# Kernel optimization log

Hardware: AMD Instinct MI355X
Metric: run time of the kernel (lower is better)

Reference implementation:

```python
import jax, jax.numpy as jnp
import numpy as np

N = 100000
E = 1600000
H = 128
G = 64  # num graphs


def setup_inputs() -> dict:
    key = jax.random.key(0)
    ks = jax.random.split(key, 20)
    s = 1.0 / np.sqrt(H)
    inp = {
        'x': jax.random.normal(ks[0], (N,), jnp.float32),
        'edge_index': jax.random.randint(ks[1], (2, E), 0, N, jnp.int32),
        'edge_attr': jax.random.normal(ks[2], (E, 1), jnp.float32),
        'batch': jnp.sort(jax.random.randint(ks[3], (N,), 0, G, jnp.int32)),
        # node/edge encoders (Linear(1, H))
        'ne_w': jax.random.normal(ks[4], (1, H), jnp.float32),
        'ne_b': jnp.zeros((H,), jnp.float32),
        'ee_w': jax.random.normal(ks[5], (1, H), jnp.float32),
        'ee_b': jnp.zeros((H,), jnp.float32),
        # conv1: internal edge lin (Linear(H,H)) + MLP (H->H->H)
        'lin1_w': jax.random.normal(ks[6], (H, H), jnp.float32) * s,
        'lin1_b': jnp.zeros((H,), jnp.float32),
        'w11': jax.random.normal(ks[7], (H, H), jnp.float32) * s,
        'b11': jnp.zeros((H,), jnp.float32),
        'w12': jax.random.normal(ks[8], (H, H), jnp.float32) * s,
        'b12': jnp.zeros((H,), jnp.float32),
        # conv2
        'lin2_w': jax.random.normal(ks[9], (H, H), jnp.float32) * s,
        'lin2_b': jnp.zeros((H,), jnp.float32),
        'w21': jax.random.normal(ks[10], (H, H), jnp.float32) * s,
        'b21': jnp.zeros((H,), jnp.float32),
        'w22': jax.random.normal(ks[11], (H, H), jnp.float32) * s,
        'b22': jnp.zeros((H,), jnp.float32),
    }
    return inp


def _gine(h, edge_index, e, lin_w, lin_b, w1, b1, w2, b2, eps=0.0):
    # message: ReLU(x_j + Lin(edge_attr)), aggregated (sum) at target nodes
    src, dst = edge_index[0], edge_index[1]
    m = jax.nn.relu(h[src] + e @ lin_w + lin_b)           # [E, H]
    agg = jax.ops.segment_sum(m, dst, num_segments=N)      # [N, H]
    z = (1.0 + eps) * h + agg
    return jax.nn.relu(z @ w1 + b1) @ w2 + b2


def reference(x, edge_index, edge_attr, batch, ne_w, ne_b, ee_w, ee_b,
              lin1_w, lin1_b, w11, b11, w12, b12,
              lin2_w, lin2_b, w21, b21, w22, b22):
    h = x.reshape(-1, 1) @ ne_w + ne_b                     # [N, H]
    e = edge_attr @ ee_w + ee_b                            # [E, H]
    h = jax.nn.relu(_gine(h, edge_index, e, lin1_w, lin1_b, w11, b11, w12, b12))
    h = jax.nn.relu(_gine(h, edge_index, e, lin2_w, lin2_b, w21, b21, w22, b22))
    # global mean pool per graph
    sums = jax.ops.segment_sum(h, batch, num_segments=G)   # [G, H]
    cnt = jax.ops.segment_sum(jnp.ones((N,), h.dtype), batch, num_segments=G)
    return sums / jnp.maximum(cnt, 1.0)[:, None]
```

## Files before the change

kernel.cpp:

```cpp
#include <hip/hip_runtime.h>

typedef unsigned short u16;
typedef unsigned int u32;
typedef __bf16 bfrag __attribute__((ext_vector_type(8)));
typedef float f32x4 __attribute__((ext_vector_type(4)));
typedef float f32x2 __attribute__((ext_vector_type(2)));

__device__ __forceinline__ u16 f2bf(float f) {
    u32 u = __float_as_uint(f);
    u32 r = (u + 0x7FFFu + ((u >> 16) & 1u)) >> 16;
    return (u16)r;
}
__device__ __forceinline__ float bf2f(u32 h) {
    return __uint_as_float(h << 16);
}

__global__ __launch_bounds__(1024) void prepack_bcount_kernel(
    const int* __restrict__ dst, int* __restrict__ bcnt, int* __restrict__ done,
    int* __restrict__ bstart, int* __restrict__ bcur, int E, int nb, int nbc,
    const float* __restrict__ w11, const float* __restrict__ w12,
    const float* __restrict__ w21, const float* __restrict__ w22,
    u16* __restrict__ hi, u16* __restrict__ lo,
    const float* __restrict__ ne_b, const float* __restrict__ ee_w, const float* __restrict__ ee_b,
    const float* __restrict__ lin1_w, const float* __restrict__ lin1_b,
    const float* __restrict__ lin2_w, const float* __restrict__ lin2_b,
    float* __restrict__ u1, float* __restrict__ C1, float* __restrict__ u2, float* __restrict__ C2)
{
    if (blockIdx.x >= (u32)nbc) {
        int pb = blockIdx.x - nbc;
        if (pb == 64) {
            int c = threadIdx.x;
            if (c < 128) {
                float s1 = 0.f, t1 = 0.f, s2 = 0.f, t2 = 0.f;
                for (int k = 0; k < 128; ++k) {
                    float w1 = lin1_w[k * 128 + c];
                    float w2 = lin2_w[k * 128 + c];
                    float ew = ee_w[k], eb = ee_b[k];
                    s1 = fmaf(ew, w1, s1); t1 = fmaf(eb, w1, t1);
                    s2 = fmaf(ew, w2, s2); t2 = fmaf(eb, w2, t2);
                }
                u1[c] = s1; C1[c] = t1 + lin1_b[c] + ne_b[c];
                u2[c] = s2; C2[c] = t2 + lin2_b[c];
            }
            return;
        }
        int which = pb >> 4;
        const float* w = (which == 0) ? w11 : (which == 1) ? w12 : (which == 2) ? w21 : w22;
        int o = (pb & 15) * 1024 + threadIdx.x;
        int j = o & 7;
        int lane = (o >> 3) & 63;
        int ct = (o >> 9) & 7;
        int ks = o >> 12;
        int k = ks * 32 + ((lane >> 4) * 8) + j;
        int c = ct * 16 + (lane & 15);
        float v = w[k * 128 + c];
        u16 h = f2bf(v);
        float vh = bf2f(h);
        u16 l = f2bf(v - vh);
        hi[which * 16384 + o] = h;
        lo[which * 16384 + o] = l;
        return;
    }

    __shared__ int h[256];
    __shared__ int is_last;
    if (threadIdx.x < 256) h[threadIdx.x] = 0;
    __syncthreads();
    int idx = blockIdx.x * 1024 + threadIdx.x;
    int e = idx * 4;
    if (e + 3 < E) {
        int4 d4 = ((const int4*)dst)[idx];
        atomicAdd(&h[d4.x >> 9], 1);
        atomicAdd(&h[d4.y >> 9], 1);
        atomicAdd(&h[d4.z >> 9], 1);
        atomicAdd(&h[d4.w >> 9], 1);
    } else {
        for (int k = e; k < E; ++k) atomicAdd(&h[dst[k] >> 9], 1);
    }
    __syncthreads();
    if (threadIdx.x < 256 && h[threadIdx.x]) atomicAdd(&bcnt[threadIdx.x], h[threadIdx.x]);
    __syncthreads();
    if (threadIdx.x == 0) {
        __threadfence();
        is_last = (atomicAdd(done, 1) == nbc - 1);
    }
    __syncthreads();
    if (!is_last) return;
    if (threadIdx.x < 256) h[threadIdx.x] = atomicAdd(&bcnt[threadIdx.x], 0);
    __syncthreads();
    __shared__ int excl[256];
    if (threadIdx.x < 64) {
        int l = threadIdx.x;
        int v0 = h[4 * l], v1 = h[4 * l + 1], v2 = h[4 * l + 2], v3 = h[4 * l + 3];
        int tot = v0 + v1 + v2 + v3;
        int run = tot;
#pragma unroll
        for (int off = 1; off < 64; off <<= 1) {
            int t = __shfl_up(run, off);
            if (l >= off) run += t;
        }
        int ex = run - tot;
        excl[4 * l] = ex;
        excl[4 * l + 1] = ex + v0;
        excl[4 * l + 2] = ex + v0 + v1;
        excl[4 * l + 3] = ex + v0 + v1 + v2;
    }
    __syncthreads();
    if (threadIdx.x < nb) {
        int ex = excl[threadIdx.x];
        bstart[threadIdx.x] = ex;
        bcur[threadIdx.x] = ex;
        if (threadIdx.x == nb - 1) bstart[nb] = ex + h[threadIdx.x];
    }
}

__global__ __launch_bounds__(1024) void bin_kernel(
    const int* __restrict__ src, const int* __restrict__ dst, const float* __restrict__ eattr,
    int* __restrict__ bucket_cursor,
    int2* __restrict__ binned, int E, int nb)
{
    __shared__ int hist[256];
    __shared__ int basel[256];
    __shared__ int gbase[256];
    __shared__ int2 stage[4096];
    __shared__ unsigned char sb[4096];
    const int tid = threadIdx.x;
    const int e0 = blockIdx.x * 4096;
    const int valid = min(4096, E - e0);

    if (tid < 256) hist[tid] = 0;
    __syncthreads();

    int d[4], s[4], a[4], rk[4];
    bool ok[4];
    const int eb = e0 + tid * 4;
    if (eb + 3 < E) {
        int4 d4 = *(const int4*)(dst + eb);
        int4 s4 = *(const int4*)(src + eb);
        int4 a4 = *(const int4*)((const int*)eattr + eb);
        d[0] = d4.x; d[1] = d4.y; d[2] = d4.z; d[3] = d4.w;
        s[0] = s4.x; s[1] = s4.y; s[2] = s4.z; s[3] = s4.w;
        a[0] = a4.x; a[1] = a4.y; a[2] = a4.z; a[3] = a4.w;
        ok[0] = ok[1] = ok[2] = ok[3] = true;
    } else {
#pragma unroll
        for (int k = 0; k < 4; ++k) {
            int e = eb + k;
            ok[k] = e < E;
            if (ok[k]) {
                d[k] = dst[e];
                s[k] = src[e];
                a[k] = __float_as_int(eattr[e]);
            }
        }
    }
#pragma unroll
    for (int k = 0; k < 4; ++k) {
        if (ok[k]) rk[k] = atomicAdd(&hist[d[k] >> 9], 1);
    }
    __syncthreads();
    if (tid < 64) {
        int l = tid;
        int v0 = hist[4 * l], v1 = hist[4 * l + 1], v2 = hist[4 * l + 2], v3 = hist[4 * l + 3];
        int tot = v0 + v1 + v2 + v3;
        int run = tot;
#pragma unroll
        for (int off = 1; off < 64; off <<= 1) {
            int t = __shfl_up(run, off);
            if (l >= off) run += t;
        }
        int ex = run - tot;
        basel[4 * l] = ex;
        basel[4 * l + 1] = ex + v0;
        basel[4 * l + 2] = ex + v0 + v1;
        basel[4 * l + 3] = ex + v0 + v1 + v2;
    }
    __syncthreads();
    if (tid < nb && hist[tid] > 0) gbase[tid] = atomicAdd(&bucket_cursor[tid], hist[tid]);
#pragma unroll
    for (int k = 0; k < 4; ++k) {
        if (ok[k]) {
            int b = d[k] >> 9;
            int pos = basel[b] + rk[k];
            stage[pos] = make_int2(s[k] | ((d[k] & 511) << 17), a[k]);
            sb[pos] = (unsigned char)b;
        }
    }
    __syncthreads();
    for (int i = tid; i < valid; i += 1024) {
        int b = (int)sb[i];
        binned[gbase[b] + (i - basel[b])] = stage[i];
    }
}

__global__ __launch_bounds__(1024) void fine_kernel(
    const int2* __restrict__ binned, const int* __restrict__ bstart,
    int* __restrict__ rowptr, int2* __restrict__ edges, int N, int nbuckets)
{
    __shared__ int hist[512];
    __shared__ int excl[512];
    const int tid = threadIdx.x;
    const int b = blockIdx.x;
    const int s0 = bstart[b], s1 = bstart[b + 1];
    if (tid < 512) hist[tid] = 0;
    __syncthreads();
    for (int i = s0 + tid; i < s1; i += 1024)
        atomicAdd(&hist[(binned[i].x >> 17) & 511], 1);
    __syncthreads();
    if (tid < 64) {
        int l = tid;
        int v[8], pre[8];
        int tot = 0;
#pragma unroll
        for (int k = 0; k < 8; ++k) { v[k] = hist[8 * l + k]; pre[k] = tot; tot += v[k]; }
        int run = tot;
#pragma unroll
        for (int off = 1; off < 64; off <<= 1) {
            int t = __shfl_up(run, off);
            if (l >= off) run += t;
        }
        int ex = run - tot;
#pragma unroll
        for (int k = 0; k < 8; ++k) excl[8 * l + k] = ex + pre[k];
    }
    __syncthreads();
    const int nbase = b << 9;
    if (tid < 512 && nbase + tid < N) rowptr[nbase + tid] = s0 + excl[tid];
    if (b == nbuckets - 1 && tid == 0) rowptr[N] = s1;
    __syncthreads();
    for (int i = s0 + tid; i < s1; i += 1024) {
        int2 ed = binned[i];
        int dlo = (ed.x >> 17) & 511;
        ed.x &= 0x1FFFF;
        int pos = atomicAdd(&excl[dlo], 1);
        edges[s0 + pos] = ed;
    }
}


__device__ __forceinline__ void p1_batch8(
    const float* __restrict__ x, const int2* __restrict__ edges, int j,
    f32x2 A, f32x2 Bv, f32x2 Cv, f32x2& acc)
{
    int2 ep = edges[j + (threadIdx.x & 7)];
    float xs[8], av[8];
#pragma unroll
    for (int t = 0; t < 8; ++t) {
        u32 s = (u32)__builtin_amdgcn_readlane(ep.x, t);
        av[t] = __int_as_float(__builtin_amdgcn_readlane(ep.y, t));
        xs[t] = *(const float*)((const char*)x + (s << 2));
    }
    const f32x2 zero = {0.f, 0.f};
#pragma unroll
    for (int t = 0; t < 8; ++t) {
        f32x2 m = __builtin_elementwise_fma((f32x2){xs[t], xs[t]}, A,
                    __builtin_elementwise_fma((f32x2){av[t], av[t]}, Bv, Cv));
        acc += __builtin_elementwise_max(m, zero);
    }
}

__device__ __forceinline__ void p1_batch8x2(
    const float* __restrict__ x, const int2* __restrict__ edges, int j0, int j1,
    f32x2 A, f32x2 Bv, f32x2 Cv, f32x2& acc0, f32x2& acc1)
{
    int2 ep0 = edges[j0 + (threadIdx.x & 7)];
    int2 ep1 = edges[j1 + (threadIdx.x & 7)];
    float xs0[8], av0[8], xs1[8], av1[8];
#pragma unroll
    for (int t = 0; t < 8; ++t) {
        u32 s = (u32)__builtin_amdgcn_readlane(ep0.x, t);
        av0[t] = __int_as_float(__builtin_amdgcn_readlane(ep0.y, t));
        xs0[t] = *(const float*)((const char*)x + (s << 2));
    }
#pragma unroll
    for (int t = 0; t < 8; ++t) {
        u32 s = (u32)__builtin_amdgcn_readlane(ep1.x, t);
        av1[t] = __int_as_float(__builtin_amdgcn_readlane(ep1.y, t));
        xs1[t] = *(const float*)((const char*)x + (s << 2));
    }
    const f32x2 zero = {0.f, 0.f};
#pragma unroll
    for (int t = 0; t < 8; ++t) {
        f32x2 m = __builtin_elementwise_fma((f32x2){xs0[t], xs0[t]}, A,
                    __builtin_elementwise_fma((f32x2){av0[t], av0[t]}, Bv, Cv));
        acc0 += __builtin_elementwise_max(m, zero);
    }
#pragma unroll
    for (int t = 0; t < 8; ++t) {
        f32x2 m = __builtin_elementwise_fma((f32x2){xs1[t], xs1[t]}, A,
                    __builtin_elementwise_fma((f32x2){av1[t], av1[t]}, Bv, Cv));
        acc1 += __builtin_elementwise_max(m, zero);
    }
}

__global__ __launch_bounds__(256) void pull1_kernel(
    const float* __restrict__ x,
    const int* __restrict__ rowptr, const int2* __restrict__ edges,
    const float* __restrict__ ne_w, const float* __restrict__ ne_b,
    const float* __restrict__ u1, const float* __restrict__ C1,
    u16* __restrict__ zb, int N)
{
    const int lane = threadIdx.x & 63;
    int pair = blockIdx.x * 4 + (threadIdx.x >> 6);
    int n0 = pair * 2;
    if (n0 >= N) return;
    const bool has1 = (n0 + 1 < N);
    f32x2 A   = *(const f32x2*)(ne_w + 2 * lane);
    f32x2 Bv  = *(const f32x2*)(u1   + 2 * lane);
    f32x2 Cv  = *(const f32x2*)(C1   + 2 * lane);
    f32x2 nbv = *(const f32x2*)(ne_b + 2 * lane);
    const f32x2 zero = {0.f, 0.f};
    int j0  = rowptr[n0];
    int je0 = rowptr[n0 + 1];
    int j1  = je0;
    int je1 = has1 ? rowptr[n0 + 2] : je0;
    float xn0 = x[n0];
    float xn1 = has1 ? x[n0 + 1] : 0.f;
    f32x2 acc0 = zero, acc1 = zero;
    while (j0 + 8 <= je0 && j1 + 8 <= je1) {
        p1_batch8x2(x, edges, j0, j1, A, Bv, Cv, acc0, acc1);
        j0 += 8; j1 += 8;
    }
    for (; j0 + 8 <= je0; j0 += 8) p1_batch8(x, edges, j0, A, Bv, Cv, acc0);
    for (; j1 + 8 <= je1; j1 += 8) p1_batch8(x, edges, j1, A, Bv, Cv, acc1);
    for (; j0 < je0; ++j0) {
        int2 ep = edges[j0];
        u32 s = (u32)__builtin_amdgcn_readfirstlane(ep.x);
        float av = __int_as_float(__builtin_amdgcn_readfirstlane(ep.y));
        float xs = *(const float*)((const char*)x + (s << 2));
        f32x2 m = __builtin_elementwise_fma((f32x2){xs, xs}, A,
                    __builtin_elementwise_fma((f32x2){av, av}, Bv, Cv));
        acc0 += __builtin_elementwise_max(m, zero);
    }
    for (; j1 < je1; ++j1) {
        int2 ep = edges[j1];
        u32 s = (u32)__builtin_amdgcn_readfirstlane(ep.x);
        float av = __int_as_float(__builtin_amdgcn_readfirstlane(ep.y));
        float xs = *(const float*)((const char*)x + (s << 2));
        f32x2 m = __builtin_elementwise_fma((f32x2){xs, xs}, A,
                    __builtin_elementwise_fma((f32x2){av, av}, Bv, Cv));
        acc1 += __builtin_elementwise_max(m, zero);
    }
    f32x2 z0 = __builtin_elementwise_fma((f32x2){xn0, xn0}, A, nbv) + acc0;
    ((u32*)(zb + (long)n0 * 128))[lane] = (u32)f2bf(z0.x) | ((u32)f2bf(z0.y) << 16);
    if (has1) {
        f32x2 z1 = __builtin_elementwise_fma((f32x2){xn1, xn1}, A, nbv) + acc1;
        ((u32*)(zb + (long)(n0 + 1) * 128))[lane] = (u32)f2bf(z1.x) | ((u32)f2bf(z1.y) << 16);
    }
}

__device__ __forceinline__ void p2_batch8(
    const u16* __restrict__ h1b, const int2* __restrict__ edges, int j,
    u32 loff, f32x2 Bv, f32x2 Cv, f32x2& acc)
{
    int2 ep = edges[j + (threadIdx.x & 7)];
    u32 hv[8];
    float av[8];
#pragma unroll
    for (int t = 0; t < 8; ++t) {
        u32 s = (u32)__builtin_amdgcn_readlane(ep.x, t);
        av[t] = __int_as_float(__builtin_amdgcn_readlane(ep.y, t));
        hv[t] = *(const u32*)((const char*)h1b + ((s << 8) | loff));
    }
    const f32x2 zero = {0.f, 0.f};
#pragma unroll
    for (int t = 0; t < 8; ++t) {
        f32x2 h = { __uint_as_float(hv[t] << 16), __uint_as_float(hv[t] & 0xFFFF0000u) };
        f32x2 m = h + __builtin_elementwise_fma((f32x2){av[t], av[t]}, Bv, Cv);
        acc += __builtin_elementwise_max(m, zero);
    }
}

__device__ __forceinline__ void p2_batch8x2(
    const u16* __restrict__ h1b, const int2* __restrict__ edges, int j0, int j1,
    u32 loff, f32x2 Bv, f32x2 Cv, f32x2& acc0, f32x2& acc1)
{
    int2 ep0 = edges[j0 + (threadIdx.x & 7)];
    int2 ep1 = edges[j1 + (threadIdx.x & 7)];
    u32 hv0[8], hv1[8];
    float av0[8], av1[8];
#pragma unroll
    for (int t = 0; t < 8; ++t) {
        u32 s = (u32)__builtin_amdgcn_readlane(ep0.x, t);
        av0[t] = __int_as_float(__builtin_amdgcn_readlane(ep0.y, t));
        hv0[t] = *(const u32*)((const char*)h1b + ((s << 8) | loff));
    }
#pragma unroll
    for (int t = 0; t < 8; ++t) {
        u32 s = (u32)__builtin_amdgcn_readlane(ep1.x, t);
        av1[t] = __int_as_float(__builtin_amdgcn_readlane(ep1.y, t));
        hv1[t] = *(const u32*)((const char*)h1b + ((s << 8) | loff));
    }
    const f32x2 zero = {0.f, 0.f};
#pragma unroll
    for (int t = 0; t < 8; ++t) {
        f32x2 h = { __uint_as_float(hv0[t] << 16), __uint_as_float(hv0[t] & 0xFFFF0000u) };
        f32x2 m = h + __builtin_elementwise_fma((f32x2){av0[t], av0[t]}, Bv, Cv);
        acc0 += __builtin_elementwise_max(m, zero);
    }
#pragma unroll
    for (int t = 0; t < 8; ++t) {
        f32x2 h = { __uint_as_float(hv1[t] << 16), __uint_as_float(hv1[t] & 0xFFFF0000u) };
        f32x2 m = h + __builtin_elementwise_fma((f32x2){av1[t], av1[t]}, Bv, Cv);
        acc1 += __builtin_elementwise_max(m, zero);
    }
}

__global__ __launch_bounds__(256) void pull2_kernel(
    const u16* __restrict__ h1b,
    const int* __restrict__ rowptr, const int2* __restrict__ edges,
    const float* __restrict__ u2, const float* __restrict__ C2,
    u16* __restrict__ zb2, int N)
{
    const int lane = threadIdx.x & 63;
    const int lane2 = 2 * lane;
    const u32 loff = (u32)lane2 * 2u;
    int pair = blockIdx.x * 4 + (threadIdx.x >> 6);
    int n0 = pair * 2;
    if (n0 >= N) return;
    const bool has1 = (n0 + 1 < N);
    f32x2 Bv = *(const f32x2*)(u2 + lane2);
    f32x2 Cv = *(const f32x2*)(C2 + lane2);
    const f32x2 zero = {0.f, 0.f};
    int j0  = rowptr[n0];
    int je0 = rowptr[n0 + 1];
    int j1  = je0;
    int je1 = has1 ? rowptr[n0 + 2] : je0;
    u32 hn0 = *(const u32*)((const char*)h1b + (((u32)n0 << 8) | loff));
    u32 hn1 = has1 ? *(const u32*)((const char*)h1b + (((u32)(n0 + 1) << 8) | loff)) : 0u;
    f32x2 acc0 = zero, acc1 = zero;
    while (j0 + 8 <= je0 && j1 + 8 <= je1) {
        p2_batch8x2(h1b, edges, j0, j1, loff, Bv, Cv, acc0, acc1);
        j0 += 8; j1 += 8;
    }
    for (; j0 + 8 <= je0; j0 += 8) p2_batch8(h1b, edges, j0, loff, Bv, Cv, acc0);
    for (; j1 + 8 <= je1; j1 += 8) p2_batch8(h1b, edges, j1, loff, Bv, Cv, acc1);
    for (; j0 < je0; ++j0) {
        int2 ep = edges[j0];
        u32 s = (u32)__builtin_amdgcn_readfirstlane(ep.x);
        float av = __int_as_float(__builtin_amdgcn_readfirstlane(ep.y));
        u32 hv = *(const u32*)((const char*)h1b + ((s << 8) | loff));
        f32x2 h = { __uint_as_float(hv << 16), __uint_as_float(hv & 0xFFFF0000u) };
        f32x2 m = h + __builtin_elementwise_fma((f32x2){av, av}, Bv, Cv);
        acc0 += __builtin_elementwise_max(m, zero);
    }
    for (; j1 < je1; ++j1) {
        int2 ep = edges[j1];
        u32 s = (u32)__builtin_amdgcn_readfirstlane(ep.x);
        float av = __int_as_float(__builtin_amdgcn_readfirstlane(ep.y));
        u32 hv = *(const u32*)((const char*)h1b + ((s << 8) | loff));
        f32x2 h = { __uint_as_float(hv << 16), __uint_as_float(hv & 0xFFFF0000u) };
        f32x2 m = h + __builtin_elementwise_fma((f32x2){av, av}, Bv, Cv);
        acc1 += __builtin_elementwise_max(m, zero);
    }
    f32x2 h0 = { __uint_as_float(hn0 << 16), __uint_as_float(hn0 & 0xFFFF0000u) };
    f32x2 z0 = h0 + acc0;
    ((u32*)(zb2 + (long)n0 * 128))[lane] = (u32)f2bf(z0.x) | ((u32)f2bf(z0.y) << 16);
    if (has1) {
        f32x2 h1 = { __uint_as_float(hn1 << 16), __uint_as_float(hn1 & 0xFFFF0000u) };
        f32x2 z1 = h1 + acc1;
        ((u32*)(zb2 + (long)(n0 + 1) * 128))[lane] = (u32)f2bf(z1.x) | ((u32)f2bf(z1.y) << 16);
    }
}

__global__ __launch_bounds__(256) void mlp_kernel(
    const u16* __restrict__ zb,
    const u16* __restrict__ w1hi, const u16* __restrict__ w1lo,
    const u16* __restrict__ w2hi, const u16* __restrict__ w2lo,
    const float* __restrict__ b1, const float* __restrict__ b2,
    u16* __restrict__ outb)
{
    __shared__ __align__(16) u16 tls[64][136];
    const int lane = threadIdx.x & 63;
    const int wv = threadIdx.x >> 6;
    const int m = lane & 15;
    const int q = lane >> 4;
    const int ko = q * 8;
    const long base_row = (long)blockIdx.x * 64;
    const int ct0 = wv * 2;

    f32x4 acc[2][4];
#pragma unroll
    for (int c = 0; c < 2; ++c)
#pragma unroll
        for (int g = 0; g < 4; ++g) acc[c][g] = (f32x4){0.f, 0.f, 0.f, 0.f};

#pragma unroll
    for (int ks = 0; ks < 4; ++ks) {
        bfrag a[4];
#pragma unroll
        for (int g = 0; g < 4; ++g)
            a[g] = *(const bfrag*)(zb + (base_row + g * 16 + m) * 128 + ks * 32 + ko);
#pragma unroll
        for (int c = 0; c < 2; ++c) {
            const int off = (((ks * 8 + ct0 + c) * 64) + lane) * 8;
            bfrag bh = *(const bfrag*)(w1hi + off);
            bfrag bl = *(const bfrag*)(w1lo + off);
#pragma unroll
            for (int g = 0; g < 4; ++g)
                acc[c][g] = __builtin_amdgcn_mfma_f32_16x16x32_bf16(a[g], bh, acc[c][g], 0, 0, 0);
#pragma unroll
            for (int g = 0; g < 4; ++g)
                acc[c][g] = __builtin_amdgcn_mfma_f32_16x16x32_bf16(a[g], bl, acc[c][g], 0, 0, 0);
        }
    }
#pragma unroll
    for (int c = 0; c < 2; ++c) {
        float bv = b1[(ct0 + c) * 16 + m];
#pragma unroll
        for (int g = 0; g < 4; ++g)
#pragma unroll
            for (int r = 0; r < 4; ++r) {
                float v = fmaxf(acc[c][g][r] + bv, 0.f);
                tls[g * 16 + q * 4 + r][(ct0 + c) * 16 + m] = f2bf(v);
            }
    }
    __syncthreads();

    f32x4 acc2[2][4];
#pragma unroll
    for (int c = 0; c < 2; ++c)
#pragma unroll
        for (int g = 0; g < 4; ++g) acc2[c][g] = (f32x4){0.f, 0.f, 0.f, 0.f};

#pragma unroll
    for (int ks = 0; ks < 4; ++ks) {
        bfrag a[4];
#pragma unroll
        for (int g = 0; g < 4; ++g)
            a[g] = *(const bfrag*)(&tls[g * 16 + m][ks * 32 + ko]);
#pragma unroll
        for (int c = 0; c < 2; ++c) {
            const int off = (((ks * 8 + ct0 + c) * 64) + lane) * 8;
            bfrag bh = *(const bfrag*)(w2hi + off);
            bfrag bl = *(const bfrag*)(w2lo + off);
#pragma unroll
            for (int g = 0; g < 4; ++g)
                acc2[c][g] = __builtin_amdgcn_mfma_f32_16x16x32_bf16(a[g], bh, acc2[c][g], 0, 0, 0);
#pragma unroll
            for (int g = 0; g < 4; ++g)
                acc2[c][g] = __builtin_amdgcn_mfma_f32_16x16x32_bf16(a[g], bl, acc2[c][g], 0, 0, 0);
        }
    }
    __syncthreads();
#pragma unroll
    for (int c = 0; c < 2; ++c) {
        float bv = b2[(ct0 + c) * 16 + m];
#pragma unroll
        for (int g = 0; g < 4; ++g)
#pragma unroll
            for (int r = 0; r < 4; ++r) {
                float v = fmaxf(acc2[c][g][r] + bv, 0.f);
                tls[g * 16 + q * 4 + r][(ct0 + c) * 16 + m] = f2bf(v);
            }
    }
    __syncthreads();
#pragma unroll
    for (int it = 0; it < 4; ++it) {
        int chunk = threadIdx.x + it * 256;
        int row = chunk >> 4;
        int c8 = (chunk & 15) * 8;
        *(uint4*)(outb + (base_row + row) * 128 + c8) = *(const uint4*)(&tls[row][c8]);
    }
}

__global__ __launch_bounds__(256) void mlp_pool_kernel(
    const u16* __restrict__ zb,
    const u16* __restrict__ w1hi, const u16* __restrict__ w1lo,
    const u16* __restrict__ w2hi, const u16* __restrict__ w2lo,
    const float* __restrict__ b1, const float* __restrict__ b2,
    const int* __restrict__ batch, float* __restrict__ poolacc, int N)
{
    __shared__ __align__(16) u16 tls[64][136];
    __shared__ int bsh[64];
    const int lane = threadIdx.x & 63;
    const int wv = threadIdx.x >> 6;
    const int m = lane & 15;
    const int q = lane >> 4;
    const int ko = q * 8;
    const long base_row = (long)blockIdx.x * 64;
    const int ct0 = wv * 2;

    if (threadIdx.x < 64) {
        long node = base_row + threadIdx.x;
        bsh[threadIdx.x] = (node < N) ? batch[node] : -1;
    }

    f32x4 acc[2][4];
#pragma unroll
    for (int c = 0; c < 2; ++c)
#pragma unroll
        for (int g = 0; g < 4; ++g) acc[c][g] = (f32x4){0.f, 0.f, 0.f, 0.f};

#pragma unroll
    for (int ks = 0; ks < 4; ++ks) {
        bfrag a[4];
#pragma unroll
        for (int g = 0; g < 4; ++g)
            a[g] = *(const bfrag*)(zb + (base_row + g * 16 + m) * 128 + ks * 32 + ko);
#pragma unroll
        for (int c = 0; c < 2; ++c) {
            const int off = (((ks * 8 + ct0 + c) * 64) + lane) * 8;
            bfrag bh = *(const bfrag*)(w1hi + off);
            bfrag bl = *(const bfrag*)(w1lo + off);
#pragma unroll
            for (int g = 0; g < 4; ++g)
                acc[c][g] = __builtin_amdgcn_mfma_f32_16x16x32_bf16(a[g], bh, acc[c][g], 0, 0, 0);
#pragma unroll
            for (int g = 0; g < 4; ++g)
                acc[c][g] = __builtin_amdgcn_mfma_f32_16x16x32_bf16(a[g], bl, acc[c][g], 0, 0, 0);
        }
    }
#pragma unroll
    for (int c = 0; c < 2; ++c) {
        float bv = b1[(ct0 + c) * 16 + m];
#pragma unroll
        for (int g = 0; g < 4; ++g)
#pragma unroll
            for (int r = 0; r < 4; ++r) {
                float v = fmaxf(acc[c][g][r] + bv, 0.f);
                tls[g * 16 + q * 4 + r][(ct0 + c) * 16 + m] = f2bf(v);
            }
    }
    __syncthreads();

    f32x4 acc2[2][4];
#pragma unroll
    for (int c = 0; c < 2; ++c)
#pragma unroll
        for (int g = 0; g < 4; ++g) acc2[c][g] = (f32x4){0.f, 0.f, 0.f, 0.f};

#pragma unroll
    for (int ks = 0; ks < 4; ++ks) {
        bfrag a[4];
#pragma unroll
        for (int g = 0; g < 4; ++g)
            a[g] = *(const bfrag*)(&tls[g * 16 + m][ks * 32 + ko]);
#pragma unroll
        for (int c = 0; c < 2; ++c) {
            const int off = (((ks * 8 + ct0 + c) * 64) + lane) * 8;
            bfrag bh = *(const bfrag*)(w2hi + off);
            bfrag bl = *(const bfrag*)(w2lo + off);
#pragma unroll
            for (int g = 0; g < 4; ++g)
                acc2[c][g] = __builtin_amdgcn_mfma_f32_16x16x32_bf16(a[g], bh, acc2[c][g], 0, 0, 0);
#pragma unroll
            for (int g = 0; g < 4; ++g)
                acc2[c][g] = __builtin_amdgcn_mfma_f32_16x16x32_bf16(a[g], bl, acc2[c][g], 0, 0, 0);
        }
    }
    __syncthreads();
#pragma unroll
    for (int c = 0; c < 2; ++c) {
        float bv = b2[(ct0 + c) * 16 + m];
#pragma unroll
        for (int g = 0; g < 4; ++g)
#pragma unroll
            for (int r = 0; r < 4; ++r) {
                float v = fmaxf(acc2[c][g][r] + bv, 0.f);
                tls[g * 16 + q * 4 + r][(ct0 + c) * 16 + m] = f2bf(v);
            }
    }
    __syncthreads();

    int c = threadIdx.x & 127;
    int half = threadIdx.x >> 7;
    int r0 = half * 32, r1 = r0 + 32;
    int cur = -1;
    float sum = 0.f;
    for (int r = r0; r < r1; ++r) {
        int g = bsh[r];
        if (g < 0) break;
        float v = bf2f((u32)tls[r][c]);
        if (g != cur) {
            if (cur >= 0) atomicAdd(&poolacc[cur * 128 + c], sum);
            sum = 0.f;
            cur = g;
        }
        sum += v;
    }
    if (cur >= 0) atomicAdd(&poolacc[cur * 128 + c], sum);
}

__global__ __launch_bounds__(128) void pool2_kernel(
    const float* __restrict__ acc, const int* __restrict__ batch,
    float* __restrict__ out, int n)
{
    int g = blockIdx.x;
    int c = threadIdx.x;
    int lo = 0, hi = n;
    while (lo < hi) { int mid = (lo + hi) >> 1; if (batch[mid] < g) lo = mid + 1; else hi = mid; }
    int s = lo;
    lo = s; hi = n;
    while (lo < hi) { int mid = (lo + hi) >> 1; if (batch[mid] < g + 1) lo = mid + 1; else hi = mid; }
    int cnt = lo - s;
    out[g * 128 + c] = acc[g * 128 + c] / (float)(cnt > 0 ? cnt : 1);
}

extern "C" void kernel_launch(void* const* d_in, const int* in_sizes, int n_in,
                              void* d_out, int out_size, void* d_ws, size_t ws_size,
                              hipStream_t stream)
{
    const float* x      = (const float*)d_in[0];
    const int*   ei     = (const int*)d_in[1];
    const float* eattr  = (const float*)d_in[2];
    const int*   batch  = (const int*)d_in[3];
    const float* ne_w   = (const float*)d_in[4];
    const float* ne_b   = (const float*)d_in[5];
    const float* ee_w   = (const float*)d_in[6];
    const float* ee_b   = (const float*)d_in[7];
    const float* lin1_w = (const float*)d_in[8];
    const float* lin1_b = (const float*)d_in[9];
    const float* w11    = (const float*)d_in[10];
    const float* b11    = (const float*)d_in[11];
    const float* w12    = (const float*)d_in[12];
    const float* b12    = (const float*)d_in[13];
    const float* lin2_w = (const float*)d_in[14];
    const float* lin2_b = (const float*)d_in[15];
    const float* w21    = (const float*)d_in[16];
    const float* b21    = (const float*)d_in[17];
    const float* w22    = (const float*)d_in[18];
    const float* b22    = (const float*)d_in[19];

    const int N = in_sizes[0];
    const int E = in_sizes[2];
    const int G = out_size / 128;
    const int Npad = ((N + 63) / 64) * 64;
    const int nb = (N + 511) >> 9;
    const int nbc = (E + 4095) / 4096;
    const int* esrc = ei;
    const int* edst = ei + E;

    char* p = (char*)d_ws;
    auto alloc = [&](size_t bytes) -> void* {
        void* r = (void*)p;
        p += (bytes + 255) & ~(size_t)255;
        return r;
    };
    float* u1 = (float*)alloc(128 * 4);
    float* C1 = (float*)alloc(128 * 4);
    float* u2 = (float*)alloc(128 * 4);
    float* C2 = (float*)alloc(128 * 4);
    int* bcnt   = (int*)alloc(1024);
    int* done   = (int*)alloc(256);
    float* poolacc = (float*)alloc((size_t)G * 128 * 4);
    int* bstart = (int*)alloc(((size_t)nb + 1) * 4);
    int* bcur   = (int*)alloc((size_t)nb * 4);
    int* rowptr = (int*)alloc(((size_t)N + 1) * 4);
    int2* edges = (int2*)alloc((size_t)E * 8);
    int2* binned = (int2*)alloc((size_t)E * 8);
    u16* whi = (u16*)alloc((size_t)4 * 16384 * 2);
    u16* wlo = (u16*)alloc((size_t)4 * 16384 * 2);
    u16* bufA = (u16*)alloc((size_t)Npad * 128 * 2);
    u16* bufB = (u16*)alloc((size_t)Npad * 128 * 2);

    size_t zbytes = (size_t)((char*)poolacc + (size_t)G * 128 * 4 - (char*)bcnt);
    hipMemsetAsync(bcnt, 0, zbytes, stream);

    prepack_bcount_kernel<<<nbc + 65, 1024, 0, stream>>>(
        edst, bcnt, done, bstart, bcur, E, nb, nbc,
        w11, w12, w21, w22, whi, wlo,
        ne_b, ee_w, ee_b, lin1_w, lin1_b, lin2_w, lin2_b, u1, C1, u2, C2);

    bin_kernel<<<nbc, 1024, 0, stream>>>(esrc, edst, eattr, bcur, binned, E, nb);
    fine_kernel<<<nb, 1024, 0, stream>>>(binned, bstart, rowptr, edges, N, nb);

    pull1_kernel<<<(N + 7) / 8, 256, 0, stream>>>(x, rowptr, edges, ne_w, ne_b, u1, C1,
                                                  bufA, N);
    mlp_kernel<<<Npad / 64, 256, 0, stream>>>(bufA, whi, wlo, whi + 16384, wlo + 16384,
                                              b11, b12, bufB);
    pull2_kernel<<<(N + 7) / 8, 256, 0, stream>>>(bufB, rowptr, edges, u2, C2, bufA, N);
    mlp_pool_kernel<<<Npad / 64, 256, 0, stream>>>(bufA, whi + 32768, wlo + 32768,
                                                   whi + 49152, wlo + 49152, b21, b22,
                                                   batch, poolacc, N);

    pool2_kernel<<<G, 128, 0, stream>>>(poolacc, batch, (float*)d_out, N);
}
```

Before: 320.8 us.

## Split each wavefront into two half-waves, one per node, with 4-wide features

The pull kernels now assign each half of a 64-lane wavefront to one of the two destination nodes. Each lane handles 4 features through 8-byte loads, where before every lane handled 2 features for both nodes. Edge indices are loaded per lane directly rather than broadcast with readlane, so the two halves gather different source rows in the same instruction. The intent is to double the bytes per gather load and remove the sequential two-node loop. The cost is wasted work when degrees differ: the inactive half still runs the tail iterations with its accumulation masked off.

New measurement: 370.0 us. 1.15x slower.

```diff
diff --git a/kernel.cpp b/kernel.cpp
--- a/kernel.cpp
+++ b/kernel.cpp
@@ -238,58 +238,34 @@
 }
 
 
-__device__ __forceinline__ void p1_batch8(
-    const float* __restrict__ x, const int2* __restrict__ edges, int j,
-    f32x2 A, f32x2 Bv, f32x2 Cv, f32x2& acc)
-{
-    int2 ep = edges[j + (threadIdx.x & 7)];
-    float xs[8], av[8];
+__device__ __forceinline__ f32x4 bf4(uint2 hv) {
+    f32x4 r;
+    r[0] = __uint_as_float(hv.x << 16);
+    r[1] = __uint_as_float(hv.x & 0xFFFF0000u);
+    r[2] = __uint_as_float(hv.y << 16);
+    r[3] = __uint_as_float(hv.y & 0xFFFF0000u);
+    return r;
+}
+
+__device__ __forceinline__ void p1_any8(
+    const float* __restrict__ x, const int2* __restrict__ edges, int jb,
+    f32x4 A, f32x4 Bv, f32x4 Cv, bool act, f32x4& acc)
+{
+    int2 ep[8];
+    float xs[8];
+#pragma unroll
+    for (int t = 0; t < 8; ++t) ep[t] = edges[jb + t];
+#pragma unroll
+    for (int t = 0; t < 8; ++t)
+        xs[t] = *(const float*)((const char*)x + (((u32)ep[t].x) << 2));
+    const f32x4 zero = {0.f, 0.f, 0.f, 0.f};
 #pragma unroll
     for (int t = 0; t < 8; ++t) {
-        u32 s = (u32)__builtin_amdgcn_readlane(ep.x, t);
-        av[t] = __int_as_float(__builtin_amdgcn_readlane(ep.y, t));
-        xs[t] = *(const float*)((const char*)x + (s << 2));
-    }
-    const f32x2 zero = {0.f, 0.f};
-#pragma unroll
-    for (int t = 0; t < 8; ++t) {
-        f32x2 m = __builtin_elementwise_fma((f32x2){xs[t], xs[t]}, A,
-                    __builtin_elementwise_fma((f32x2){av[t], av[t]}, Bv, Cv));
-        acc += __builtin_elementwise_max(m, zero);
-    }
-}
-
-__device__ __forceinline__ void p1_batch8x2(
-    const float* __restrict__ x, const int2* __restrict__ edges, int j0, int j1,
-    f32x2 A, f32x2 Bv, f32x2 Cv, f32x2& acc0, f32x2& acc1)
-{
-    int2 ep0 = edges[j0 + (threadIdx.x & 7)];
-    int2 ep1 = edges[j1 + (threadIdx.x & 7)];
-    float xs0[8], av0[8], xs1[8], av1[8];
-#pragma unroll
-    for (int t = 0; t < 8; ++t) {
-        u32 s = (u32)__builtin_amdgcn_readlane(ep0.x, t);
-        av0[t] = __int_as_float(__builtin_amdgcn_readlane(ep0.y, t));
-        xs0[t] = *(const float*)((const char*)x + (s << 2));
-    }
-#pragma unroll
-    for (int t = 0; t < 8; ++t) {
-        u32 s = (u32)__builtin_amdgcn_readlane(ep1.x, t);
-        av1[t] = __int_as_float(__builtin_amdgcn_readlane(ep1.y, t));
-        xs1[t] = *(const float*)((const char*)x + (s << 2));
-    }
-    const f32x2 zero = {0.f, 0.f};
-#pragma unroll
-    for (int t = 0; t < 8; ++t) {
-        f32x2 m = __builtin_elementwise_fma((f32x2){xs0[t], xs0[t]}, A,
-                    __builtin_elementwise_fma((f32x2){av0[t], av0[t]}, Bv, Cv));
-        acc0 += __builtin_elementwise_max(m, zero);
-    }
-#pragma unroll
-    for (int t = 0; t < 8; ++t) {
-        f32x2 m = __builtin_elementwise_fma((f32x2){xs1[t], xs1[t]}, A,
-                    __builtin_elementwise_fma((f32x2){av1[t], av1[t]}, Bv, Cv));
-        acc1 += __builtin_elementwise_max(m, zero);
+        float av = __int_as_float(ep[t].y);
+        f32x4 m = __builtin_elementwise_fma((f32x4){xs[t], xs[t], xs[t], xs[t]}, A,
+                    __builtin_elementwise_fma((f32x4){av, av, av, av}, Bv, Cv));
+        m = __builtin_elementwise_max(m, zero);
+        if (act) acc += m;
     }
 }
 
@@ -301,108 +277,76 @@
     u16* __restrict__ zb, int N)
 {
     const int lane = threadIdx.x & 63;
+    const int half = lane >> 5;
+    const int cl = lane & 31;
+    const u32 loff = (u32)cl * 8u;
     int pair = blockIdx.x * 4 + (threadIdx.x >> 6);
     int n0 = pair * 2;
     if (n0 >= N) return;
     const bool has1 = (n0 + 1 < N);
-    f32x2 A   = *(const f32x2*)(ne_w + 2 * lane);
-    f32x2 Bv  = *(const f32x2*)(u1   + 2 * lane);
-    f32x2 Cv  = *(const f32x2*)(C1   + 2 * lane);
-    f32x2 nbv = *(const f32x2*)(ne_b + 2 * lane);
-    const f32x2 zero = {0.f, 0.f};
+    f32x4 A   = *(const f32x4*)(ne_w + cl * 4);
+    f32x4 Bv  = *(const f32x4*)(u1   + cl * 4);
+    f32x4 Cv  = *(const f32x4*)(C1   + cl * 4);
+    f32x4 nbv = *(const f32x4*)(ne_b + cl * 4);
+    const f32x4 zero = {0.f, 0.f, 0.f, 0.f};
     int j0  = rowptr[n0];
     int je0 = rowptr[n0 + 1];
     int j1  = je0;
     int je1 = has1 ? rowptr[n0 + 2] : je0;
-    float xn0 = x[n0];
-    float xn1 = has1 ? x[n0 + 1] : 0.f;
-    f32x2 acc0 = zero, acc1 = zero;
+    const int nself = half ? (has1 ? n0 + 1 : n0) : n0;
+    float xn = x[nself];
+    f32x4 acc = zero;
     while (j0 + 8 <= je0 && j1 + 8 <= je1) {
-        p1_batch8x2(x, edges, j0, j1, A, Bv, Cv, acc0, acc1);
+        int jb = half ? j1 : j0;
+        p1_any8(x, edges, jb, A, Bv, Cv, true, acc);
         j0 += 8; j1 += 8;
     }
-    for (; j0 + 8 <= je0; j0 += 8) p1_batch8(x, edges, j0, A, Bv, Cv, acc0);
-    for (; j1 + 8 <= je1; j1 += 8) p1_batch8(x, edges, j1, A, Bv, Cv, acc1);
+    while (j0 + 8 <= je0) { p1_any8(x, edges, j0, A, Bv, Cv, half == 0, acc); j0 += 8; }
+    while (j1 + 8 <= je1) { p1_any8(x, edges, j1, A, Bv, Cv, half == 1, acc); j1 += 8; }
     for (; j0 < je0; ++j0) {
         int2 ep = edges[j0];
-        u32 s = (u32)__builtin_amdgcn_readfirstlane(ep.x);
-        float av = __int_as_float(__builtin_amdgcn_readfirstlane(ep.y));
-        float xs = *(const float*)((const char*)x + (s << 2));
-        f32x2 m = __builtin_elementwise_fma((f32x2){xs, xs}, A,
-                    __builtin_elementwise_fma((f32x2){av, av}, Bv, Cv));
-        acc0 += __builtin_elementwise_max(m, zero);
+        float xs = *(const float*)((const char*)x + (((u32)ep.x) << 2));
+        float av = __int_as_float(ep.y);
+        f32x4 m = __builtin_elementwise_fma((f32x4){xs, xs, xs, xs}, A,
+                    __builtin_elementwise_fma((f32x4){av, av, av, av}, Bv, Cv));
+        m = __builtin_elementwise_max(m, zero);
+        if (half == 0) acc += m;
     }
     for (; j1 < je1; ++j1) {
         int2 ep = edges[j1];
-        u32 s = (u32)__builtin_amdgcn_readfirstlane(ep.x);
-        float av = __int_as_float(__builtin_amdgcn_readfirstlane(ep.y));
-        float xs = *(const float*)((const char*)x + (s << 2));
-        f32x2 m = __builtin_elementwise_fma((f32x2){xs, xs}, A,
-                    __builtin_elementwise_fma((f32x2){av, av}, Bv, Cv));
-        acc1 += __builtin_elementwise_max(m, zero);
-    }
-    f32x2 z0 = __builtin_elementwise_fma((f32x2){xn0, xn0}, A, nbv) + acc0;
-    ((u32*)(zb + (long)n0 * 128))[lane] = (u32)f2bf(z0.x) | ((u32)f2bf(z0.y) << 16);
-    if (has1) {
-        f32x2 z1 = __builtin_elementwise_fma((f32x2){xn1, xn1}, A, nbv) + acc1;
-        ((u32*)(zb + (long)(n0 + 1) * 128))[lane] = (u32)f2bf(z1.x) | ((u32)f2bf(z1.y) << 16);
-    }
-}
-
-__device__ __forceinline__ void p2_batch8(
-    const u16* __restrict__ h1b, const int2* __restrict__ edges, int j,
-    u32 loff, f32x2 Bv, f32x2 Cv, f32x2& acc)
-{
-    int2 ep = edges[j + (threadIdx.x & 7)];
-    u32 hv[8];
-    float av[8];
+        float xs = *(const float*)((const char*)x + (((u32)ep.x) << 2));
+        float av = __int_as_float(ep.y);
+        f32x4 m = __builtin_elementwise_fma((f32x4){xs, xs, xs, xs}, A,
+                    __builtin_elementwise_fma((f32x4){av, av, av, av}, Bv, Cv));
+        m = __builtin_elementwise_max(m, zero);
+        if (half == 1) acc += m;
+    }
+    f32x4 z = __builtin_elementwise_fma((f32x4){xn, xn, xn, xn}, A, nbv) + acc;
+    uint2 outp;
+    outp.x = (u32)f2bf(z[0]) | ((u32)f2bf(z[1]) << 16);
+    outp.y = (u32)f2bf(z[2]) | ((u32)f2bf(z[3]) << 16);
+    if (half == 0 || has1)
+        *(uint2*)((char*)zb + (((u32)nself) << 8) + loff) = outp;
+}
+
+__device__ __forceinline__ void p2_any8(
+    const u16* __restrict__ h1b, const int2* __restrict__ edges, int jb, u32 loff,
+    f32x4 Bv, f32x4 Cv, bool act, f32x4& acc)
+{
+    int2 ep[8];
+    uint2 hv[8];
+#pragma unroll
+    for (int t = 0; t < 8; ++t) ep[t] = edges[jb + t];
+#pragma unroll
+    for (int t = 0; t < 8; ++t)
+        hv[t] = *(const uint2*)((const char*)h1b + ((((u32)ep[t].x) << 8) | loff));
+    const f32x4 zero = {0.f, 0.f, 0.f, 0.f};
 #pragma unroll
     for (int t = 0; t < 8; ++t) {
-        u32 s = (u32)__builtin_amdgcn_readlane(ep.x, t);
-        av[t] = __int_as_float(__builtin_amdgcn_readlane(ep.y, t));
-        hv[t] = *(const u32*)((const char*)h1b + ((s << 8) | loff));
-    }
-    const f32x2 zero = {0.f, 0.f};
-#pragma unroll
-    for (int t = 0; t < 8; ++t) {
-        f32x2 h = { __uint_as_float(hv[t] << 16), __uint_as_float(hv[t] & 0xFFFF0000u) };
-        f32x2 m = h + __builtin_elementwise_fma((f32x2){av[t], av[t]}, Bv, Cv);
-        acc += __builtin_elementwise_max(m, zero);
-    }
-}
-
-__device__ __forceinline__ void p2_batch8x2(
-    const u16* __restrict__ h1b, const int2* __restrict__ edges, int j0, int j1,
-    u32 loff, f32x2 Bv, f32x2 Cv, f32x2& acc0, f32x2& acc1)
-{
-    int2 ep0 = edges[j0 + (threadIdx.x & 7)];
-    int2 ep1 = edges[j1 + (threadIdx.x & 7)];
-    u32 hv0[8], hv1[8];
-    float av0[8], av1[8];
-#pragma unroll
-    for (int t = 0; t < 8; ++t) {
-        u32 s = (u32)__builtin_amdgcn_readlane(ep0.x, t);
-        av0[t] = __int_as_float(__builtin_amdgcn_readlane(ep0.y, t));
-        hv0[t] = *(const u32*)((const char*)h1b + ((s << 8) | loff));
-    }
-#pragma unroll
-    for (int t = 0; t < 8; ++t) {
-        u32 s = (u32)__builtin_amdgcn_readlane(ep1.x, t);
-        av1[t] = __int_as_float(__builtin_amdgcn_readlane(ep1.y, t));
-        hv1[t] = *(const u32*)((const char*)h1b + ((s << 8) | loff));
-    }
-    const f32x2 zero = {0.f, 0.f};
-#pragma unroll
-    for (int t = 0; t < 8; ++t) {
-        f32x2 h = { __uint_as_float(hv0[t] << 16), __uint_as_float(hv0[t] & 0xFFFF0000u) };
-        f32x2 m = h + __builtin_elementwise_fma((f32x2){av0[t], av0[t]}, Bv, Cv);
-        acc0 += __builtin_elementwise_max(m, zero);
-    }
-#pragma unroll
-    for (int t = 0; t < 8; ++t) {
-        f32x2 h = { __uint_as_float(hv1[t] << 16), __uint_as_float(hv1[t] & 0xFFFF0000u) };
-        f32x2 m = h + __builtin_elementwise_fma((f32x2){av1[t], av1[t]}, Bv, Cv);
-        acc1 += __builtin_elementwise_max(m, zero);
+        float av = __int_as_float(ep[t].y);
+        f32x4 m = bf4(hv[t]) + __builtin_elementwise_fma((f32x4){av, av, av, av}, Bv, Cv);
+        m = __builtin_elementwise_max(m, zero);
+        if (act) acc += m;
     }
 }
 
@@ -413,54 +357,52 @@
     u16* __restrict__ zb2, int N)
 {
     const int lane = threadIdx.x & 63;
-    const int lane2 = 2 * lane;
-    const u32 loff = (u32)lane2 * 2u;
+    const int half = lane >> 5;
+    const int cl = lane & 31;
+    const u32 loff = (u32)cl * 8u;
     int pair = blockIdx.x * 4 + (threadIdx.x >> 6);
     int n0 = pair * 2;
     if (n0 >= N) return;
     const bool has1 = (n0 + 1 < N);
-    f32x2 Bv = *(const f32x2*)(u2 + lane2);
-    f32x2 Cv = *(const f32x2*)(C2 + lane2);
-    const f32x2 zero = {0.f, 0.f};
+    f32x4 Bv = *(const f32x4*)(u2 + cl * 4);
+    f32x4 Cv = *(const f32x4*)(C2 + cl * 4);
+    const f32x4 zero = {0.f, 0.f, 0.f, 0.f};
     int j0  = rowptr[n0];
     int je0 = rowptr[n0 + 1];
     int j1  = je0;
     int je1 = has1 ? rowptr[n0 + 2] : je0;
-    u32 hn0 = *(const u32*)((const char*)h1b + (((u32)n0 << 8) | loff));
-    u32 hn1 = has1 ? *(const u32*)((const char*)h1b + (((u32)(n0 + 1) << 8) | loff)) : 0u;
-    f32x2 acc0 = zero, acc1 = zero;
+    const int nself = half ? (has1 ? n0 + 1 : n0) : n0;
+    uint2 hnp = *(const uint2*)((const char*)h1b + (((u32)nself << 8) | loff));
+    f32x4 acc = zero;
     while (j0 + 8 <= je0 && j1 + 8 <= je1) {
-        p2_batch8x2(h1b, edges, j0, j1, loff, Bv, Cv, acc0, acc1);
+        int jb = half ? j1 : j0;
+        p2_any8(h1b, edges, jb, loff, Bv, Cv, true, acc);
         j0 += 8; j1 += 8;
     }
-    for (; j0 + 8 <= je0; j0 += 8) p2_batch8(h1b, edges, j0, loff, Bv, Cv, acc0);
-    for (; j1 + 8 <= je1; j1 += 8) p2_batch8(h1b, edges, j1, loff, Bv, Cv, acc1);
+    while (j0 + 8 <= je0) { p2_any8(h1b, edges, j0, loff, Bv, Cv, half == 0, acc); j0 += 8; }
+    while (j1 + 8 <= je1) { p2_any8(h1b, edges, j1, loff, Bv, Cv, half == 1, acc); j1 += 8; }
     for (; j0 < je0; ++j0) {
         int2 ep = edges[j0];
-        u32 s = (u32)__builtin_amdgcn_readfirstlane(ep.x);
-        float av = __int_as_float(__builtin_amdgcn_readfirstlane(ep.y));
-        u32 hv = *(const u32*)((const char*)h1b + ((s << 8) | loff));
-        f32x2 h = { __uint_as_float(hv << 16), __uint_as_float(hv & 0xFFFF0000u) };
-        f32x2 m = h + __builtin_elementwise_fma((f32x2){av, av}, Bv, Cv);
-        acc0 += __builtin_elementwise_max(m, zero);
+        uint2 hv = *(const uint2*)((const char*)h1b + ((((u32)ep.x) << 8) | loff));
+        float av = __int_as_float(ep.y);
+        f32x4 m = bf4(hv) + __builtin_elementwise_fma((f32x4){av, av, av, av}, Bv, Cv);
+        m = __builtin_elementwise_max(m, zero);
+        if (half == 0) acc += m;
     }
     for (; j1 < je1; ++j1) {
         int2 ep = edges[j1];
-        u32 s = (u32)__builtin_amdgcn_readfirstlane(ep.x);
-        float av = __int_as_float(__builtin_amdgcn_readfirstlane(ep.y));
-        u32 hv = *(const u32*)((const char*)h1b + ((s << 8) | loff));
-        f32x2 h = { __uint_as_float(hv << 16), __uint_as_float(hv & 0xFFFF0000u) };
-        f32x2 m = h + __builtin_elementwise_fma((f32x2){av, av}, Bv, Cv);
-        acc1 += __builtin_elementwise_max(m, zero);
-    }
-    f32x2 h0 = { __uint_as_float(hn0 << 16), __uint_as_float(hn0 & 0xFFFF0000u) };
-    f32x2 z0 = h0 + acc0;
-    ((u32*)(zb2 + (long)n0 * 128))[lane] = (u32)f2bf(z0.x) | ((u32)f2bf(z0.y) << 16);
-    if (has1) {
-        f32x2 h1 = { __uint_as_float(hn1 << 16), __uint_as_float(hn1 & 0xFFFF0000u) };
-        f32x2 z1 = h1 + acc1;
-        ((u32*)(zb2 + (long)(n0 + 1) * 128))[lane] = (u32)f2bf(z1.x) | ((u32)f2bf(z1.y) << 16);
-    }
+        uint2 hv = *(const uint2*)((const char*)h1b + ((((u32)ep.x) << 8) | loff));
+        float av = __int_as_float(ep.y);
+        f32x4 m = bf4(hv) + __builtin_elementwise_fma((f32x4){av, av, av, av}, Bv, Cv);
+        m = __builtin_elementwise_max(m, zero);
+        if (half == 1) acc += m;
+    }
+    f32x4 z = bf4(hnp) + acc;
+    uint2 outp;
+    outp.x = (u32)f2bf(z[0]) | ((u32)f2bf(z[1]) << 16);
+    outp.y = (u32)f2bf(z[2]) | ((u32)f2bf(z[3]) << 16);
+    if (half == 0 || has1)
+        *(uint2*)((char*)zb2 + (((u32)nself) << 8) + loff) = outp;
 }
 
 __global__ __launch_bounds__(256) void mlp_kernel(
```
